# Kernel optimization log

Measured on AMD Instinct MI355X. Metric: run time of the kernel, lower is better.

Reference implementation:

```python
import jax, jax.numpy as jnp
import numpy as np

N_NODES = 50000


def setup_inputs() -> dict:
    key = jax.random.key(0)
    k1, k2, k3, k4, k5 = jax.random.split(key, 5)
    E = 1600000
    features = jax.random.normal(k1, (N_NODES, 256), dtype=jnp.float32)
    weight = jax.random.normal(k2, (256, 64), dtype=jnp.float32) * (1.0 / np.sqrt(256))
    edge_row = jax.random.randint(k3, (E,), 0, N_NODES, dtype=jnp.int64 if jax.config.jax_enable_x64 else jnp.int32)
    edge_col = jax.random.randint(k4, (E,), 0, N_NODES, dtype=jnp.int64 if jax.config.jax_enable_x64 else jnp.int32)
    edge_weight = jax.random.uniform(k5, (E,), dtype=jnp.float32)
    return {
        "features": features,
        "weight": weight,
        "edge_row": edge_row,
        "edge_col": edge_col,
        "edge_weight": edge_weight,
        "active": 1,
    }


def reference(features, weight, edge_row, edge_col, edge_weight, active):
    # support = features @ W  -- dense projection [N, out]
    support = features @ weight
    # output = spmm(adj, support): gather source rows, scale by edge weight,
    # scatter-add into destination rows (COO SpMM).
    msgs = support[edge_col] * edge_weight[:, None]           # [E, out]
    output = jax.ops.segment_sum(msgs, edge_row, num_segments=N_NODES)  # [N, out]
    if active:
        output = jnp.tanh(output)
    return output
```

## Files before the change

### kernel.cpp

```cpp
#include <hip/hip_runtime.h>
#include <hip/hip_fp16.h>
#include <math.h>

#define N_NODES 50000
#define IN_F 256
#define OUT_F 64
#define NBUCK 391
#define CHUNK 4096
#define CAPB 4608

typedef unsigned int uint;
typedef __attribute__((ext_vector_type(8))) short short8v;
typedef __attribute__((ext_vector_type(4))) short short4v;
typedef __attribute__((ext_vector_type(4))) float f32x4;


__device__ __forceinline__ short bf16_trunc(float f) {
    return (short)(__float_as_uint(f) >> 16);
}
__device__ __forceinline__ float bf16_tof(short s) {
    return __uint_as_float(((uint)(unsigned short)s) << 16);
}
__device__ __forceinline__ short bf16_rne(float f) {
    uint u = __float_as_uint(f);
    uint r = u + 0x7FFF + ((u >> 16) & 1);
    return (short)(r >> 16);
}

__global__ __launch_bounds__(256) void wprep_kernel(const float* __restrict__ W,
                                                    short* __restrict__ Whi,
                                                    short* __restrict__ Wlo,
                                                    int* __restrict__ gcnt) {
    const int t = threadIdx.x;
    const int k0 = blockIdx.x * 32;
    if (blockIdx.x == 0) {
        for (int i = t; i < NBUCK; i += 256) gcnt[i] = 0;
    }

    __shared__ float buf[32][65];
    for (int i = t; i < 32 * 64; i += 256) {
        int kk = i >> 6, c = i & 63;
        buf[kk][c] = W[(k0 + kk) * 64 + c];
    }
    __syncthreads();
    {
        int c = t & 63, g = t >> 6;
        short8v vh, vl;
        for (int j = 0; j < 8; ++j) {
            float f = buf[g * 8 + j][c];
            short h = bf16_trunc(f);
            vh[j] = h;
            vl[j] = bf16_rne(f - bf16_tof(h));
        }
        *(short8v*)&Whi[c * IN_F + k0 + g * 8] = vh;
        *(short8v*)&Wlo[c * IN_F + k0 + g * 8] = vl;
    }
}

__global__ __launch_bounds__(256) void gemm_kernel(const float* __restrict__ feat,
                                                   const short* __restrict__ Whi,
                                                   const short* __restrict__ Wlo,
                                                   __half* __restrict__ sup) {
    __shared__ short lds[15360];
    short* As_hi = lds;
    short* As_lo = lds + 5120;
    short* Bs_hi = lds + 10240;
    short* Bs_lo = lds + 12800;

    const int t = threadIdx.x;
    const int row0 = blockIdx.x * 128;
    const int l = t & 63;
    const int lr = l & 15;
    const int lk = (l >> 4) * 8;
    const int wrow = (t >> 6) * 32;

    const int ar = t >> 1, aq = t & 1;
    int gr = row0 + ar; if (gr >= N_NODES) gr = N_NODES - 1;
    const float4* asrc = (const float4*)(feat + (size_t)gr * IN_F);
    const int bc = t >> 2, bp = t & 3;

    f32x4 acc[2][4];
#pragma unroll
    for (int m = 0; m < 2; ++m)
#pragma unroll
        for (int nn = 0; nn < 4; ++nn) acc[m][nn] = (f32x4)(0.f);

    for (int ch = 0; ch < 8; ++ch) {
        float4 av[4];
#pragma unroll
        for (int i = 0; i < 4; ++i) av[i] = asrc[ch * 8 + aq * 4 + i];
        short8v bh = *(const short8v*)(Whi + bc * IN_F + ch * 32 + bp * 8);
        short8v bl = *(const short8v*)(Wlo + bc * IN_F + ch * 32 + bp * 8);

        __syncthreads();
#pragma unroll
        for (int i = 0; i < 4; ++i) {
            float fx[4] = {av[i].x, av[i].y, av[i].z, av[i].w};
            short4v h4, l4;
#pragma unroll
            for (int j = 0; j < 4; ++j) {
                short h = bf16_trunc(fx[j]);
                h4[j] = h;
                l4[j] = bf16_rne(fx[j] - bf16_tof(h));
            }
            *(short4v*)&As_hi[ar * 40 + aq * 16 + i * 4] = h4;
            *(short4v*)&As_lo[ar * 40 + aq * 16 + i * 4] = l4;
        }
        *(short8v*)&Bs_hi[bc * 40 + bp * 8] = bh;
        *(short8v*)&Bs_lo[bc * 40 + bp * 8] = bl;
        __syncthreads();

        short8v ah[2], al[2], wh[4], wl[4];
#pragma unroll
        for (int m = 0; m < 2; ++m) {
            ah[m] = *(short8v*)&As_hi[(wrow + m * 16 + lr) * 40 + lk];
            al[m] = *(short8v*)&As_lo[(wrow + m * 16 + lr) * 40 + lk];
        }
#pragma unroll
        for (int nn = 0; nn < 4; ++nn) {
            wh[nn] = *(short8v*)&Bs_hi[(nn * 16 + lr) * 40 + lk];
            wl[nn] = *(short8v*)&Bs_lo[(nn * 16 + lr) * 40 + lk];
        }
#pragma unroll
        for (int m = 0; m < 2; ++m)
#pragma unroll
            for (int nn = 0; nn < 4; ++nn) {
                acc[m][nn] = __builtin_amdgcn_mfma_f32_16x16x32_bf16(ah[m], wh[nn], acc[m][nn], 0, 0, 0);
                acc[m][nn] = __builtin_amdgcn_mfma_f32_16x16x32_bf16(ah[m], wl[nn], acc[m][nn], 0, 0, 0);
                acc[m][nn] = __builtin_amdgcn_mfma_f32_16x16x32_bf16(al[m], wh[nn], acc[m][nn], 0, 0, 0);
            }
    }

    __syncthreads();
    short* sup_s = lds;
#pragma unroll
    for (int m = 0; m < 2; ++m) {
        int rr = wrow + m * 16 + (l >> 4) * 4;
#pragma unroll
        for (int nn = 0; nn < 4; ++nn) {
            int cc = nn * 16 + lr;
#pragma unroll
            for (int j = 0; j < 4; ++j) {
                __half h = __float2half(acc[m][nn][j]);
                sup_s[(rr + j) * 64 + cc] = *(short*)&h;
            }
        }
    }
    __syncthreads();
    {
        int r = t >> 1, sg = (t & 1) * 32;
        int grow = row0 + r;
        if (grow < N_NODES) {
            const uint4* s4 = (const uint4*)&sup_s[r * 64 + sg];
            uint4* d4 = (uint4*)(sup + (size_t)grow * OUT_F + sg);
            d4[0] = s4[0];
            d4[1] = s4[1];
            d4[2] = s4[2];
            d4[3] = s4[3];
        }
    }
}

__global__ __launch_bounds__(1024) void bin_kernel(const int* __restrict__ erow,
                                                   const int* __restrict__ ecol,
                                                   const float* __restrict__ ew,
                                                   int* __restrict__ gcnt,
                                                   int2* __restrict__ ecw, int E) {
    __shared__ int   h[NBUCK];
    __shared__ uint  pkst[CHUNK];
    __shared__ float wst[CHUNK];
    const int t = threadIdx.x;
    const int base = blockIdx.x * CHUNK;

    for (int i = t; i < NBUCK; i += 1024) h[i] = 0;
    __syncthreads();

    const int e4 = base + 4 * t;
    if (e4 + 3 < E) {
        int4   r4 = *(const int4*)(erow + e4);
        int4   c4 = *(const int4*)(ecol + e4);
        float4 w4 = *(const float4*)(ew + e4);
        pkst[4 * t + 0] = ((uint)r4.x << 16) | (uint)c4.x;
        pkst[4 * t + 1] = ((uint)r4.y << 16) | (uint)c4.y;
        pkst[4 * t + 2] = ((uint)r4.z << 16) | (uint)c4.z;
        pkst[4 * t + 3] = ((uint)r4.w << 16) | (uint)c4.w;
        *(float4*)(wst + 4 * t) = w4;
        atomicAdd(&h[r4.x >> 7], 1);
        atomicAdd(&h[r4.y >> 7], 1);
        atomicAdd(&h[r4.z >> 7], 1);
        atomicAdd(&h[r4.w >> 7], 1);
    } else {
        for (int k = 0; k < 4; ++k) {
            int e = e4 + k;
            if (e < E) {
                int row = erow[e];
                pkst[4 * t + k] = ((uint)row << 16) | (uint)ecol[e];
                wst[4 * t + k] = ew[e];
                atomicAdd(&h[row >> 7], 1);
            }
        }
    }
    __syncthreads();

    for (int i = t; i < NBUCK; i += 1024) {
        int c = h[i];
        if (c > 0) h[i] = atomicAdd(&gcnt[i], c);
    }
    __syncthreads();

    const int lim = min(CHUNK, E - base);
    for (int i = t; i < lim; i += 1024) {
        uint  pk = pkst[i];
        float w  = wst[i];
        int b = (int)(pk >> 23);
        int pos = atomicAdd(&h[b], 1);
        if (pos < CAPB)
            ecw[(size_t)b * CAPB + pos] =
                make_int2((int)(pk & 0x7FFFFF), __float_as_int(w));
    }
}

__global__ __launch_bounds__(1024) void reduce_kernel(const __half* __restrict__ sup,
                                                      const int* __restrict__ gcnt,
                                                      const int2* __restrict__ ecw,
                                                      const int* __restrict__ active,
                                                      float* __restrict__ out) {
    __shared__ int2 stA[CAPB];
    __shared__ int2 stB[CAPB];
    __shared__ int h[128];
    __shared__ int sc[128];
    __shared__ int cur[128];
    const int t = threadIdx.x;
    const int b = blockIdx.x;

    int n = gcnt[b]; if (n > CAPB) n = CAPB;
    const int2* eptr = ecw + (size_t)b * CAPB;

    if (t < 128) h[t] = 0;
    __syncthreads();

    for (int i = t; i < n; i += 1024) {
        int2 d = eptr[i];
        stA[i] = d;
        atomicAdd(&h[(d.x >> 16) & 127], 1);
    }
    __syncthreads();

    if (t < 128) sc[t] = h[t];
    __syncthreads();
    for (int off = 1; off < 128; off <<= 1) {
        int u = (t < 128 && t >= off) ? sc[t - off] : 0;
        __syncthreads();
        if (t < 128) sc[t] += u;
        __syncthreads();
    }
    if (t < 128) cur[t] = sc[t] - h[t];
    __syncthreads();

    for (int i = t; i < n; i += 1024) {
        int2 d = stA[i];
        int r = (d.x >> 16) & 127;
        int pos = atomicAdd(&cur[r], 1);
        stB[pos] = make_int2(d.x & 0xFFFF, d.y);
    }
    __syncthreads();

    const int wid  = t >> 6;
    const int lane = t & 63;
    const int hl   = lane & 31;
    const bool hi  = lane >= 32;
    const int act  = *active;

    for (int r = wid; r < 128; r += 16) {
        int row = b * 128 + r;
        if (row >= N_NODES) break;
        const int s = sc[r] - h[r];
        const int e = sc[r];
        float ax = 0.f, ay = 0.f;
        int j = s;
        for (; j + 8 <= e; j += 8) {
#pragma unroll
            for (int q = 0; q < 4; ++q) {
                int2 pa = stB[j + 2 * q];
                int2 pb = stB[j + 2 * q + 1];
                int   col = hi ? pb.x : pa.x;
                float w   = __int_as_float(hi ? pb.y : pa.y);
                const __half2* hp = (const __half2*)(sup + ((size_t)col << 6));
                float2 v = __half22float2(hp[hl]);
                ax += w * v.x;
                ay += w * v.y;
            }
        }
        for (; j + 2 <= e; j += 2) {
            int2 pa = stB[j];
            int2 pb = stB[j + 1];
            int   col = hi ? pb.x : pa.x;
            float w   = __int_as_float(hi ? pb.y : pa.y);
            const __half2* hp = (const __half2*)(sup + ((size_t)col << 6));
            float2 v = __half22float2(hp[hl]);
            ax += w * v.x;
            ay += w * v.y;
        }
        if (j < e) {
            int2 pa = stB[j];
            int   col = pa.x;
            float w   = hi ? 0.f : __int_as_float(pa.y);
            const __half2* hp = (const __half2*)(sup + ((size_t)col << 6));
            float2 v = __half22float2(hp[hl]);
            ax += w * v.x;
            ay += w * v.y;
        }

        ax += __shfl_xor(ax, 32, 64);
        ay += __shfl_xor(ay, 32, 64);

        if (!hi) {
            if (act) { ax = tanhf(ax); ay = tanhf(ay); }
            *(float2*)&out[((size_t)row << 6) + 2 * hl] = make_float2(ax, ay);
        }
    }
}

extern "C" void kernel_launch(void* const* d_in, const int* in_sizes, int n_in,
                              void* d_out, int out_size, void* d_ws, size_t ws_size,
                              hipStream_t stream) {
    const float* feat = (const float*)d_in[0];
    const float* W    = (const float*)d_in[1];
    const int*   erow = (const int*)d_in[2];
    const int*   ecol = (const int*)d_in[3];
    const float* ew   = (const float*)d_in[4];
    const int*   act  = (const int*)d_in[5];
    float* out = (float*)d_out;

    const int E = in_sizes[2];
    const int G = (E + CHUNK - 1) / CHUNK;

    char* ws = (char*)d_ws;
    __half* sup  = (__half*)ws; ws += (size_t)N_NODES * OUT_F * 2;
    int2*   ecw  = (int2*)ws;   ws += (size_t)NBUCK * CAPB * 8;
    int*    gcnt = (int*)ws;    ws += ((size_t)NBUCK * 4 + 15) & ~15;
    short*  Whi  = (short*)ws;  ws += (size_t)OUT_F * IN_F * 2;
    short*  Wlo  = (short*)ws;  ws += (size_t)OUT_F * IN_F * 2;

    wprep_kernel<<<8, 256, 0, stream>>>(W, Whi, Wlo, gcnt);
    gemm_kernel<<<(N_NODES + 127) / 128, 256, 0, stream>>>(feat, Whi, Wlo, sup);
    bin_kernel<<<G, 1024, 0, stream>>>(erow, ecol, ew, gcnt, ecw, E);
    reduce_kernel<<<NBUCK, 1024, 0, stream>>>(sup, gcnt, ecw, act, out);
}
```

Baseline: 173.8 us.

## Fuse GEMM and edge binning into one launch; add work-queue reduce

After: 194.9 us. 1.12x slower.

```diff
diff --git a/kernel.cpp b/kernel.cpp
--- a/kernel.cpp
+++ b/kernel.cpp
@@ -8,6 +8,9 @@
 #define NBUCK 391
 #define CHUNK 4096
 #define CAPB 4608
+#define GEMM_ROWS 256
+#define GEMM_BLOCKS ((N_NODES + GEMM_ROWS - 1) / GEMM_ROWS)
+#define RED_BLOCKS 256
 
 typedef unsigned int uint;
 typedef __attribute__((ext_vector_type(8))) short short8v;
@@ -34,7 +37,7 @@
     const int t = threadIdx.x;
     const int k0 = blockIdx.x * 32;
     if (blockIdx.x == 0) {
-        for (int i = t; i < NBUCK; i += 256) gcnt[i] = 0;
+        for (int i = t; i < NBUCK + 1; i += 256) gcnt[i] = 0;
     }
 
     __shared__ float buf[32][65];
@@ -57,166 +60,171 @@
     }
 }
 
-__global__ __launch_bounds__(256) void gemm_kernel(const float* __restrict__ feat,
-                                                   const short* __restrict__ Whi,
-                                                   const short* __restrict__ Wlo,
-                                                   __half* __restrict__ sup) {
-    __shared__ short lds[15360];
-    short* As_hi = lds;
-    short* As_lo = lds + 5120;
-    short* Bs_hi = lds + 10240;
-    short* Bs_lo = lds + 12800;
-
+__global__ __launch_bounds__(1024) void fused_kernel(const float* __restrict__ feat,
+                                                     const short* __restrict__ Whi,
+                                                     const short* __restrict__ Wlo,
+                                                     __half* __restrict__ sup,
+                                                     const int* __restrict__ erow,
+                                                     const int* __restrict__ ecol,
+                                                     const float* __restrict__ ew,
+                                                     int* __restrict__ gcnt,
+                                                     int2* __restrict__ ecw,
+                                                     int E, int G) {
+    __shared__ char ldsraw[51200];
     const int t = threadIdx.x;
-    const int row0 = blockIdx.x * 128;
-    const int l = t & 63;
-    const int lr = l & 15;
-    const int lk = (l >> 4) * 8;
-    const int wrow = (t >> 6) * 32;
-
-    const int ar = t >> 1, aq = t & 1;
-    int gr = row0 + ar; if (gr >= N_NODES) gr = N_NODES - 1;
-    const float4* asrc = (const float4*)(feat + (size_t)gr * IN_F);
-    const int bc = t >> 2, bp = t & 3;
-
-    f32x4 acc[2][4];
-#pragma unroll
-    for (int m = 0; m < 2; ++m)
-#pragma unroll
-        for (int nn = 0; nn < 4; ++nn) acc[m][nn] = (f32x4)(0.f);
-
-    for (int ch = 0; ch < 8; ++ch) {
-        float4 av[4];
-#pragma unroll
-        for (int i = 0; i < 4; ++i) av[i] = asrc[ch * 8 + aq * 4 + i];
-        short8v bh = *(const short8v*)(Whi + bc * IN_F + ch * 32 + bp * 8);
-        short8v bl = *(const short8v*)(Wlo + bc * IN_F + ch * 32 + bp * 8);
-
-        __syncthreads();
-#pragma unroll
-        for (int i = 0; i < 4; ++i) {
-            float fx[4] = {av[i].x, av[i].y, av[i].z, av[i].w};
-            short4v h4, l4;
-#pragma unroll
-            for (int j = 0; j < 4; ++j) {
-                short h = bf16_trunc(fx[j]);
-                h4[j] = h;
-                l4[j] = bf16_rne(fx[j] - bf16_tof(h));
-            }
-            *(short4v*)&As_hi[ar * 40 + aq * 16 + i * 4] = h4;
-            *(short4v*)&As_lo[ar * 40 + aq * 16 + i * 4] = l4;
-        }
-        *(short8v*)&Bs_hi[bc * 40 + bp * 8] = bh;
-        *(short8v*)&Bs_lo[bc * 40 + bp * 8] = bl;
-        __syncthreads();
-
-        short8v ah[2], al[2], wh[4], wl[4];
-#pragma unroll
-        for (int m = 0; m < 2; ++m) {
-            ah[m] = *(short8v*)&As_hi[(wrow + m * 16 + lr) * 40 + lk];
-            al[m] = *(short8v*)&As_lo[(wrow + m * 16 + lr) * 40 + lk];
-        }
-#pragma unroll
-        for (int nn = 0; nn < 4; ++nn) {
-            wh[nn] = *(short8v*)&Bs_hi[(nn * 16 + lr) * 40 + lk];
-            wl[nn] = *(short8v*)&Bs_lo[(nn * 16 + lr) * 40 + lk];
-        }
-#pragma unroll
-        for (int m = 0; m < 2; ++m)
+
+    if ((int)blockIdx.x < G) {
+        int*   h    = (int*)ldsraw;
+        uint*  pkst = (uint*)(ldsraw + 1600);
+        float* wst  = (float*)(ldsraw + 1600 + 16384);
+        const int base = blockIdx.x * CHUNK;
+
+        for (int i = t; i < NBUCK; i += 1024) h[i] = 0;
+        __syncthreads();
+
+        const int e4 = base + 4 * t;
+        if (e4 + 3 < E) {
+            int4   r4 = *(const int4*)(erow + e4);
+            int4   c4 = *(const int4*)(ecol + e4);
+            float4 w4 = *(const float4*)(ew + e4);
+            pkst[4 * t + 0] = ((uint)r4.x << 16) | (uint)c4.x;
+            pkst[4 * t + 1] = ((uint)r4.y << 16) | (uint)c4.y;
+            pkst[4 * t + 2] = ((uint)r4.z << 16) | (uint)c4.z;
+            pkst[4 * t + 3] = ((uint)r4.w << 16) | (uint)c4.w;
+            *(float4*)(wst + 4 * t) = w4;
+            atomicAdd(&h[r4.x >> 7], 1);
+            atomicAdd(&h[r4.y >> 7], 1);
+            atomicAdd(&h[r4.z >> 7], 1);
+            atomicAdd(&h[r4.w >> 7], 1);
+        } else {
+            for (int k = 0; k < 4; ++k) {
+                int e = e4 + k;
+                if (e < E) {
+                    int row = erow[e];
+                    pkst[4 * t + k] = ((uint)row << 16) | (uint)ecol[e];
+                    wst[4 * t + k] = ew[e];
+                    atomicAdd(&h[row >> 7], 1);
+                }
+            }
+        }
+        __syncthreads();
+
+        for (int i = t; i < NBUCK; i += 1024) {
+            int c = h[i];
+            if (c > 0) h[i] = atomicAdd(&gcnt[i], c);
+        }
+        __syncthreads();
+
+        const int lim = min(CHUNK, E - base);
+        for (int i = t; i < lim; i += 1024) {
+            uint  pk = pkst[i];
+            float w  = wst[i];
+            int b = (int)(pk >> 23);
+            int pos = atomicAdd(&h[b], 1);
+            if (pos < CAPB)
+                ecw[(size_t)b * CAPB + pos] =
+                    make_int2((int)(pk & 0x7FFFFF), __float_as_int(w));
+        }
+    } else {
+        short* As_hi = (short*)ldsraw;
+        short* As_lo = As_hi + 10240;
+        short* Bs_hi = As_lo + 10240;
+        short* Bs_lo = Bs_hi + 2560;
+
+        const int row0 = ((int)blockIdx.x - G) * GEMM_ROWS;
+        const int l = t & 63;
+        const int wid = t >> 6;
+        const int lr = l & 15;
+        const int lk = (l >> 4) * 8;
+        const int wrow = wid * 16;
+
+        const int ar = t >> 2, aq = t & 3;
+        int gr = row0 + ar; if (gr >= N_NODES) gr = N_NODES - 1;
+        const float4* asrc = (const float4*)(feat + (size_t)gr * IN_F);
+        const int bc = t >> 4, bq = t & 15;
+        const uint* bsrch = (const uint*)(Whi + bc * IN_F);
+        const uint* bsrcl = (const uint*)(Wlo + bc * IN_F);
+
+        f32x4 acc[4];
+#pragma unroll
+        for (int nn = 0; nn < 4; ++nn) acc[nn] = (f32x4)(0.f);
+
+        float4 av0 = asrc[aq * 2];
+        float4 av1 = asrc[aq * 2 + 1];
+        uint bh = bsrch[bq];
+        uint bl = bsrcl[bq];
+
+        for (int ch = 0; ch < 8; ++ch) {
+            {
+                float fx[8] = {av0.x, av0.y, av0.z, av0.w, av1.x, av1.y, av1.z, av1.w};
+                short4v h4a, l4a, h4b, l4b;
+#pragma unroll
+                for (int j = 0; j < 4; ++j) {
+                    short hh = bf16_trunc(fx[j]);
+                    h4a[j] = hh;
+                    l4a[j] = bf16_rne(fx[j] - bf16_tof(hh));
+                }
+#pragma unroll
+                for (int j = 0; j < 4; ++j) {
+                    short hh = bf16_trunc(fx[4 + j]);
+                    h4b[j] = hh;
+                    l4b[j] = bf16_rne(fx[4 + j] - bf16_tof(hh));
+                }
+                *(short4v*)&As_hi[ar * 40 + aq * 8]     = h4a;
+                *(short4v*)&As_hi[ar * 40 + aq * 8 + 4] = h4b;
+                *(short4v*)&As_lo[ar * 40 + aq * 8]     = l4a;
+                *(short4v*)&As_lo[ar * 40 + aq * 8 + 4] = l4b;
+                *(uint*)&Bs_hi[bc * 40 + bq * 2] = bh;
+                *(uint*)&Bs_lo[bc * 40 + bq * 2] = bl;
+            }
+            __syncthreads();
+
+            if (ch < 7) {
+                av0 = asrc[(ch + 1) * 8 + aq * 2];
+                av1 = asrc[(ch + 1) * 8 + aq * 2 + 1];
+                bh = bsrch[(ch + 1) * 16 + bq];
+                bl = bsrcl[(ch + 1) * 16 + bq];
+            }
+
+            short8v ah = *(short8v*)&As_hi[(wrow + lr) * 40 + lk];
+            short8v al = *(short8v*)&As_lo[(wrow + lr) * 40 + lk];
+            short8v wh[4], wl[4];
 #pragma unroll
             for (int nn = 0; nn < 4; ++nn) {
-                acc[m][nn] = __builtin_amdgcn_mfma_f32_16x16x32_bf16(ah[m], wh[nn], acc[m][nn], 0, 0, 0);
-                acc[m][nn] = __builtin_amdgcn_mfma_f32_16x16x32_bf16(ah[m], wl[nn], acc[m][nn], 0, 0, 0);
-                acc[m][nn] = __builtin_amdgcn_mfma_f32_16x16x32_bf16(al[m], wh[nn], acc[m][nn], 0, 0, 0);
-            }
-    }
-
-    __syncthreads();
-    short* sup_s = lds;
-#pragma unroll
-    for (int m = 0; m < 2; ++m) {
-        int rr = wrow + m * 16 + (l >> 4) * 4;
+                wh[nn] = *(short8v*)&Bs_hi[(nn * 16 + lr) * 40 + lk];
+                wl[nn] = *(short8v*)&Bs_lo[(nn * 16 + lr) * 40 + lk];
+            }
+#pragma unroll
+            for (int nn = 0; nn < 4; ++nn) {
+                acc[nn] = __builtin_amdgcn_mfma_f32_16x16x32_bf16(ah, wh[nn], acc[nn], 0, 0, 0);
+                acc[nn] = __builtin_amdgcn_mfma_f32_16x16x32_bf16(ah, wl[nn], acc[nn], 0, 0, 0);
+                acc[nn] = __builtin_amdgcn_mfma_f32_16x16x32_bf16(al, wh[nn], acc[nn], 0, 0, 0);
+            }
+            __syncthreads();
+        }
+
+        short* sup_s = (short*)ldsraw;
 #pragma unroll
         for (int nn = 0; nn < 4; ++nn) {
             int cc = nn * 16 + lr;
+            int rr = wrow + (l >> 4) * 4;
 #pragma unroll
             for (int j = 0; j < 4; ++j) {
-                __half h = __float2half(acc[m][nn][j]);
-                sup_s[(rr + j) * 64 + cc] = *(short*)&h;
-            }
-        }
-    }
-    __syncthreads();
-    {
-        int r = t >> 1, sg = (t & 1) * 32;
-        int grow = row0 + r;
-        if (grow < N_NODES) {
-            const uint4* s4 = (const uint4*)&sup_s[r * 64 + sg];
-            uint4* d4 = (uint4*)(sup + (size_t)grow * OUT_F + sg);
-            d4[0] = s4[0];
-            d4[1] = s4[1];
-            d4[2] = s4[2];
-            d4[3] = s4[3];
-        }
-    }
-}
-
-__global__ __launch_bounds__(1024) void bin_kernel(const int* __restrict__ erow,
-                                                   const int* __restrict__ ecol,
-                                                   const float* __restrict__ ew,
-                                                   int* __restrict__ gcnt,
-                                                   int2* __restrict__ ecw, int E) {
-    __shared__ int   h[NBUCK];
-    __shared__ uint  pkst[CHUNK];
-    __shared__ float wst[CHUNK];
-    const int t = threadIdx.x;
-    const int base = blockIdx.x * CHUNK;
-
-    for (int i = t; i < NBUCK; i += 1024) h[i] = 0;
-    __syncthreads();
-
-    const int e4 = base + 4 * t;
-    if (e4 + 3 < E) {
-        int4   r4 = *(const int4*)(erow + e4);
-        int4   c4 = *(const int4*)(ecol + e4);
-        float4 w4 = *(const float4*)(ew + e4);
-        pkst[4 * t + 0] = ((uint)r4.x << 16) | (uint)c4.x;
-        pkst[4 * t + 1] = ((uint)r4.y << 16) | (uint)c4.y;
-        pkst[4 * t + 2] = ((uint)r4.z << 16) | (uint)c4.z;
-        pkst[4 * t + 3] = ((uint)r4.w << 16) | (uint)c4.w;
-        *(float4*)(wst + 4 * t) = w4;
-        atomicAdd(&h[r4.x >> 7], 1);
-        atomicAdd(&h[r4.y >> 7], 1);
-        atomicAdd(&h[r4.z >> 7], 1);
-        atomicAdd(&h[r4.w >> 7], 1);
-    } else {
-        for (int k = 0; k < 4; ++k) {
-            int e = e4 + k;
-            if (e < E) {
-                int row = erow[e];
-                pkst[4 * t + k] = ((uint)row << 16) | (uint)ecol[e];
-                wst[4 * t + k] = ew[e];
-                atomicAdd(&h[row >> 7], 1);
-            }
-        }
-    }
-    __syncthreads();
-
-    for (int i = t; i < NBUCK; i += 1024) {
-        int c = h[i];
-        if (c > 0) h[i] = atomicAdd(&gcnt[i], c);
-    }
-    __syncthreads();
-
-    const int lim = min(CHUNK, E - base);
-    for (int i = t; i < lim; i += 1024) {
-        uint  pk = pkst[i];
-        float w  = wst[i];
-        int b = (int)(pk >> 23);
-        int pos = atomicAdd(&h[b], 1);
-        if (pos < CAPB)
-            ecw[(size_t)b * CAPB + pos] =
-                make_int2((int)(pk & 0x7FFFFF), __float_as_int(w));
+                __half hv = __float2half(acc[nn][j]);
+                sup_s[(rr + j) * 64 + cc] = *(short*)&hv;
+            }
+        }
+        __syncthreads();
+        {
+            int r = t >> 2;
+            int grow = row0 + r;
+            if (grow < N_NODES) {
+                const uint4* s4 = (const uint4*)&sup_s[r * 64 + (t & 3) * 16];
+                uint4* d4 = (uint4*)(sup + (size_t)grow * OUT_F + (t & 3) * 16);
+                d4[0] = s4[0];
+                d4[1] = s4[1];
+            }
+        }
     }
 }
 
@@ -224,65 +232,79 @@
                                                       const int* __restrict__ gcnt,
                                                       const int2* __restrict__ ecw,
                                                       const int* __restrict__ active,
-                                                      float* __restrict__ out) {
+                                                      float* __restrict__ out,
+                                                      int* __restrict__ nextq) {
     __shared__ int2 stA[CAPB];
     __shared__ int2 stB[CAPB];
     __shared__ int h[128];
     __shared__ int sc[128];
     __shared__ int cur[128];
+    __shared__ int bshare;
     const int t = threadIdx.x;
-    const int b = blockIdx.x;
-
-    int n = gcnt[b]; if (n > CAPB) n = CAPB;
-    const int2* eptr = ecw + (size_t)b * CAPB;
-
-    if (t < 128) h[t] = 0;
-    __syncthreads();
-
-    for (int i = t; i < n; i += 1024) {
-        int2 d = eptr[i];
-        stA[i] = d;
-        atomicAdd(&h[(d.x >> 16) & 127], 1);
-    }
-    __syncthreads();
-
-    if (t < 128) sc[t] = h[t];
-    __syncthreads();
-    for (int off = 1; off < 128; off <<= 1) {
-        int u = (t < 128 && t >= off) ? sc[t - off] : 0;
-        __syncthreads();
-        if (t < 128) sc[t] += u;
-        __syncthreads();
-    }
-    if (t < 128) cur[t] = sc[t] - h[t];
-    __syncthreads();
-
-    for (int i = t; i < n; i += 1024) {
-        int2 d = stA[i];
-        int r = (d.x >> 16) & 127;
-        int pos = atomicAdd(&cur[r], 1);
-        stB[pos] = make_int2(d.x & 0xFFFF, d.y);
-    }
-    __syncthreads();
+    const int act = *active;
 
     const int wid  = t >> 6;
     const int lane = t & 63;
     const int hl   = lane & 31;
     const bool hi  = lane >= 32;
-    const int act  = *active;
-
-    for (int r = wid; r < 128; r += 16) {
-        int row = b * 128 + r;
-        if (row >= N_NODES) break;
-        const int s = sc[r] - h[r];
-        const int e = sc[r];
-        float ax = 0.f, ay = 0.f;
-        int j = s;
-        for (; j + 8 <= e; j += 8) {
-#pragma unroll
-            for (int q = 0; q < 4; ++q) {
-                int2 pa = stB[j + 2 * q];
-                int2 pb = stB[j + 2 * q + 1];
+
+    int b = blockIdx.x;
+    while (b < NBUCK) {
+        int n = gcnt[b]; if (n > CAPB) n = CAPB;
+        const int2* eptr = ecw + (size_t)b * CAPB;
+
+        if (t < 128) h[t] = 0;
+        __syncthreads();
+
+        for (int i = t; i < n; i += 1024) {
+            int2 d = eptr[i];
+            stA[i] = d;
+            atomicAdd(&h[(d.x >> 16) & 127], 1);
+        }
+        __syncthreads();
+
+        if (t < 128) sc[t] = h[t];
+        __syncthreads();
+        for (int off = 1; off < 128; off <<= 1) {
+            int u = (t < 128 && t >= off) ? sc[t - off] : 0;
+            __syncthreads();
+            if (t < 128) sc[t] += u;
+            __syncthreads();
+        }
+        if (t < 128) cur[t] = sc[t] - h[t];
+        __syncthreads();
+
+        for (int i = t; i < n; i += 1024) {
+            int2 d = stA[i];
+            int r = (d.x >> 16) & 127;
+            int pos = atomicAdd(&cur[r], 1);
+            stB[pos] = make_int2(d.x & 0xFFFF, d.y);
+        }
+        __syncthreads();
+
+        for (int r = wid; r < 128; r += 16) {
+            int row = b * 128 + r;
+            if (row >= N_NODES) break;
+            const int s = sc[r] - h[r];
+            const int e = sc[r];
+            float ax = 0.f, ay = 0.f;
+            int j = s;
+            for (; j + 8 <= e; j += 8) {
+#pragma unroll
+                for (int q = 0; q < 4; ++q) {
+                    int2 pa = stB[j + 2 * q];
+                    int2 pb = stB[j + 2 * q + 1];
+                    int   col = hi ? pb.x : pa.x;
+                    float w   = __int_as_float(hi ? pb.y : pa.y);
+                    const __half2* hp = (const __half2*)(sup + ((size_t)col << 6));
+                    float2 v = __half22float2(hp[hl]);
+                    ax += w * v.x;
+                    ay += w * v.y;
+                }
+            }
+            for (; j + 2 <= e; j += 2) {
+                int2 pa = stB[j];
+                int2 pb = stB[j + 1];
                 int   col = hi ? pb.x : pa.x;
                 float w   = __int_as_float(hi ? pb.y : pa.y);
                 const __half2* hp = (const __half2*)(sup + ((size_t)col << 6));
@@ -290,34 +312,29 @@
                 ax += w * v.x;
                 ay += w * v.y;
             }
-        }
-        for (; j + 2 <= e; j += 2) {
-            int2 pa = stB[j];
-            int2 pb = stB[j + 1];
-            int   col = hi ? pb.x : pa.x;
-            float w   = __int_as_float(hi ? pb.y : pa.y);
-            const __half2* hp = (const __half2*)(sup + ((size_t)col << 6));
-            float2 v = __half22float2(hp[hl]);
-            ax += w * v.x;
-            ay += w * v.y;
-        }
-        if (j < e) {
-            int2 pa = stB[j];
-            int   col = pa.x;
-            float w   = hi ? 0.f : __int_as_float(pa.y);
-            const __half2* hp = (const __half2*)(sup + ((size_t)col << 6));
-            float2 v = __half22float2(hp[hl]);
-            ax += w * v.x;
-            ay += w * v.y;
-        }
-
-        ax += __shfl_xor(ax, 32, 64);
-        ay += __shfl_xor(ay, 32, 64);
-
-        if (!hi) {
-            if (act) { ax = tanhf(ax); ay = tanhf(ay); }
-            *(float2*)&out[((size_t)row << 6) + 2 * hl] = make_float2(ax, ay);
-        }
+            if (j < e) {
+                int2 pa = stB[j];
+                int   col = pa.x;
+                float w   = hi ? 0.f : __int_as_float(pa.y);
+                const __half2* hp = (const __half2*)(sup + ((size_t)col << 6));
+                float2 v = __half22float2(hp[hl]);
+                ax += w * v.x;
+                ay += w * v.y;
+            }
+
+            ax += __shfl_xor(ax, 32, 64);
+            ay += __shfl_xor(ay, 32, 64);
+
+            if (!hi) {
+                if (act) { ax = tanhf(ax); ay = tanhf(ay); }
+                *(float2*)&out[((size_t)row << 6) + 2 * hl] = make_float2(ax, ay);
+            }
+        }
+
+        __syncthreads();
+        if (t == 0) bshare = RED_BLOCKS + atomicAdd(nextq, 1);
+        __syncthreads();
+        b = bshare;
     }
 }
 
@@ -338,12 +355,13 @@
     char* ws = (char*)d_ws;
     __half* sup  = (__half*)ws; ws += (size_t)N_NODES * OUT_F * 2;
     int2*   ecw  = (int2*)ws;   ws += (size_t)NBUCK * CAPB * 8;
-    int*    gcnt = (int*)ws;    ws += ((size_t)NBUCK * 4 + 15) & ~15;
+    int*    gcnt = (int*)ws;    ws += ((size_t)(NBUCK + 1) * 4 + 15) & ~15;
     short*  Whi  = (short*)ws;  ws += (size_t)OUT_F * IN_F * 2;
     short*  Wlo  = (short*)ws;  ws += (size_t)OUT_F * IN_F * 2;
+    int*    nextq = gcnt + NBUCK;
 
     wprep_kernel<<<8, 256, 0, stream>>>(W, Whi, Wlo, gcnt);
-    gemm_kernel<<<(N_NODES + 127) / 128, 256, 0, stream>>>(feat, Whi, Wlo, sup);
-    bin_kernel<<<G, 1024, 0, stream>>>(erow, ecol, ew, gcnt, ecw, E);
-    reduce_kernel<<<NBUCK, 1024, 0, stream>>>(sup, gcnt, ecw, act, out);
-}
+    fused_kernel<<<G + GEMM_BLOCKS, 1024, 0, stream>>>(feat, Whi, Wlo, sup,
+                                                       erow, ecol, ew, gcnt, ecw, E, G);
+    reduce_kernel<<<RED_BLOCKS, 1024, 0, stream>>>(sup, gcnt, ecw, act, out, nextq);
+}
```
